# Optimization experiments

Hardware: AMD Instinct MI355X
Metric: run time of the kernel (lower is better)

The kernel has to match this reference:

```python
import jax, jax.numpy as jnp
import numpy as np

NUM_QUBITS = 4
QUANTUM_DEPTH = 2
BATCH = 1048576

# Hadamard matrix
_H = jnp.asarray(np.array([[1.0, 1.0], [1.0, -1.0]]) / np.sqrt(2.0), jnp.complex64)

# PauliZ sign table: signs[w, k] = +/-1 for basis state k on wire w (wire 0 = most significant axis)
_idx = np.arange(16)
_SIGNS = jnp.asarray(np.stack([1.0 - 2.0 * ((_idx >> (NUM_QUBITS - 1 - w)) & 1) for w in range(NUM_QUBITS)]), jnp.float32)  # (4,16)


def _apply_1q(state, U, w):
    # state: (B,2,2,2,2); apply 2x2 U on wire w
    a = 1 + w
    s = jnp.moveaxis(state, a, -1)
    s = s @ U.T  # new_j = sum_i U[j,i] * s[..., i]
    return jnp.moveaxis(s, -1, a)


def _apply_rz(state, theta, w):
    # diagonal RZ(theta) = diag(e^{-i t/2}, e^{i t/2}), theta: (B,)
    ph = jnp.exp(1j * jnp.stack([-theta / 2, theta / 2], axis=-1).astype(jnp.complex64))  # (B,2)
    shape = [state.shape[0], 1, 1, 1, 1]
    shape[1 + w] = 2
    return state * ph.reshape(shape)


def _cnot(state, c, t):
    ca, ta = 1 + c, 1 + t
    s0 = jnp.take(state, 0, axis=ca)
    s1 = jnp.take(state, 1, axis=ca)
    s1 = jnp.flip(s1, axis=ta if ta < ca else ta - 1)
    return jnp.stack([s0, s1], axis=ca)


def _ry_matrix(theta):
    c, s = jnp.cos(theta / 2), jnp.sin(theta / 2)
    return jnp.stack([jnp.stack([c, -s]), jnp.stack([s, c])]).astype(jnp.complex64)


def _simulate(inputs, params):
    B = inputs.shape[0]
    state = jnp.zeros((B, 2, 2, 2, 2), jnp.complex64).at[:, 0, 0, 0, 0].set(1.0)
    # feature map: H on all wires, RZ(inputs[:, w]), CNOT chain
    for w in range(NUM_QUBITS):
        state = _apply_1q(state, _H, w)
    for w in range(NUM_QUBITS):
        state = _apply_rz(state, inputs[:, w], w)
    for w in range(NUM_QUBITS - 1):
        state = _cnot(state, w, w + 1)
    # variational circuit
    for layer in range(QUANTUM_DEPTH):
        for w in range(NUM_QUBITS):
            state = _apply_1q(state, _ry_matrix(params[layer, w]), w)
        for w in range(NUM_QUBITS - 1):
            state = _cnot(state, w, w + 1)
        state = _cnot(state, NUM_QUBITS - 1, 0)
    probs = jnp.abs(state.reshape(B, 16)) ** 2  # (B,16) float32
    return probs @ _SIGNS.T  # (B,4) expvals of PauliZ per wire


def setup_inputs() -> dict:
    key = jax.random.key(0)
    k1, k2 = jax.random.split(key)
    inputs = jax.random.normal(k1, (BATCH, NUM_QUBITS), jnp.float32)
    params = jax.random.normal(k2, (QUANTUM_DEPTH, NUM_QUBITS), jnp.float32) * 0.1
    return {"inputs": inputs, "params": params}


def reference(inputs, params):
    return _simulate(inputs, params)
```

## Files before the change

### kernel.cpp

```cpp
#include <hip/hip_runtime.h>


typedef float v2f __attribute__((ext_vector_type(2)));

__global__ __launch_bounds__(256) void qsim_kernel(
    const float* __restrict__ inputs,
    const float* __restrict__ params,
    float* __restrict__ out,
    int B)
{
    int b = blockIdx.x * blockDim.x + threadIdx.x;
    if (b >= B) return;

    const float4 x4 = reinterpret_cast<const float4*>(inputs)[b];

    float cw[4], sw[4];
    __sincosf(0.5f * x4.x, &sw[0], &cw[0]);
    __sincosf(0.5f * x4.y, &sw[1], &cw[1]);
    __sincosf(0.5f * x4.z, &sw[2], &cw[2]);
    __sincosf(0.5f * x4.w, &sw[3], &cw[3]);

    v2f a[16];
    a[0] = (v2f){0.25f * cw[3], -0.25f * sw[3]};
    a[1] = (v2f){0.25f * cw[3],  0.25f * sw[3]};

    #pragma unroll
    for (int lvl = 0; lvl < 3; ++lvl) {
        const int w = 2 - lvl;
        const int st = 2 << lvl;
        const float c = cw[w], s = sw[w];
        #pragma unroll
        for (int j = 0; j < 8; ++j) {
            if (j < st) {
                const v2f v  = a[j];
                const v2f cv = v * c;
                const v2f sp = (v2f){-v.y, v.x} * s;
                a[j]      = cv - sp;
                a[j + st] = cv + sp;
            }
        }
    }

    auto cnot = [&](int cm, int tm) {
        #pragma unroll
        for (int j = 0; j < 16; ++j) {
            if ((j & cm) && !(j & tm)) {
                const int k = j | tm;
                v2f tmp = a[j]; a[j] = a[k]; a[k] = tmp;
            }
        }
    };

    auto ry = [&](int m, float c, float s) {
        #pragma unroll
        for (int j = 0; j < 16; ++j) {
            if (!(j & m)) {
                const int k = j | m;
                const v2f a0 = a[j], a1 = a[k];
                a[j] = a0 * c - a1 * s;
                a[k] = a0 * s + a1 * c;
            }
        }
    };

    cnot(8, 4); cnot(4, 2); cnot(2, 1);

    #pragma unroll
    for (int l = 0; l < 2; ++l) {
        float cp[4], sp[4];
        #pragma unroll
        for (int w = 0; w < 4; ++w)
            __sincosf(0.5f * params[l * 4 + w], &sp[w], &cp[w]);
        ry(8, cp[0], sp[0]);
        ry(4, cp[1], sp[1]);
        ry(2, cp[2], sp[2]);
        ry(1, cp[3], sp[3]);
        cnot(8, 4); cnot(4, 2); cnot(2, 1); cnot(1, 8);
    }

    v2f q[16];
    #pragma unroll
    for (int k = 0; k < 16; ++k) q[k] = a[k] * a[k];

    v2f t[8], o3v = (v2f){0.f, 0.f};
    #pragma unroll
    for (int j = 0; j < 8; ++j) {
        t[j] = q[2*j] + q[2*j+1];
        o3v += q[2*j] - q[2*j+1];
    }
    v2f u[4], o2v = (v2f){0.f, 0.f};
    #pragma unroll
    for (int j = 0; j < 4; ++j) {
        u[j] = t[2*j] + t[2*j+1];
        o2v += t[2*j] - t[2*j+1];
    }
    const v2f o1v = (u[0] - u[1]) + (u[2] - u[3]);
    const v2f o0v = (u[0] + u[1]) - (u[2] + u[3]);

    reinterpret_cast<float4*>(out)[b] =
        make_float4(o0v.x + o0v.y, o1v.x + o1v.y, o2v.x + o2v.y, o3v.x + o3v.y);
}

extern "C" void kernel_launch(void* const* d_in, const int* in_sizes, int n_in,
                              void* d_out, int out_size, void* d_ws, size_t ws_size,
                              hipStream_t stream) {
    const float* inputs = (const float*)d_in[0];
    const float* params = (const float*)d_in[1];
    float* out = (float*)d_out;
    const int B = in_sizes[0] / 4;
    const int threads = 256;
    const int blocks = (B + threads - 1) / threads;
    qsim_kernel<<<blocks, threads, 0, stream>>>(inputs, params, out, B);
}
```

Before: 79.75 us.

## Precompute parameter-only circuit into Fourier coefficient table, evaluate per-sample as trig polynomial

Adds a single-block prep kernel that builds the 16x16 unitary of the parameter-only part of the circuit. From it, the prep kernel derives a table of 81 float4 Fourier coefficients for the PauliZ expectations as functions of the input phases. The main kernel then computes per-sample phase products and sums coefficient-weighted cosines, instead of simulating the full 16-amplitude state per thread. This trades state-vector simulation work for an extra small launch and table reads from global memory. The prep kernel is still valid per call, since it reads params each time.

Result: faster. 75.99 us (-4.7%).

```diff
diff --git a/kernel.cpp b/kernel.cpp
--- a/kernel.cpp
+++ b/kernel.cpp
@@ -3,102 +3,133 @@
 
 typedef float v2f __attribute__((ext_vector_type(2)));
 
-__global__ __launch_bounds__(256) void qsim_kernel(
+__global__ void qprep_kernel(const float* __restrict__ params, float* __restrict__ tab) {
+    __shared__ float V[16][16];
+    __shared__ float4 T[81];
+    const int tid = threadIdx.x;
+    if (tid < 81) T[tid] = make_float4(0.f, 0.f, 0.f, 0.f);
+    if (tid < 16) {
+        float col[16];
+        #pragma unroll
+        for (int j = 0; j < 16; ++j) col[j] = (j == tid) ? 1.f : 0.f;
+        auto cnot = [&](int cm, int tm) {
+            #pragma unroll
+            for (int j = 0; j < 16; ++j)
+                if ((j & cm) && !(j & tm)) { int k = j | tm; float t0 = col[j]; col[j] = col[k]; col[k] = t0; }
+        };
+        auto ry = [&](int m, float c, float s) {
+            #pragma unroll
+            for (int j = 0; j < 16; ++j)
+                if (!(j & m)) { int k = j | m; float a0 = col[j], a1 = col[k]; col[j] = c*a0 - s*a1; col[k] = s*a0 + c*a1; }
+        };
+        cnot(8, 4); cnot(4, 2); cnot(2, 1);
+        #pragma unroll
+        for (int l = 0; l < 2; ++l) {
+            float cp[4], sp[4];
+            #pragma unroll
+            for (int w = 0; w < 4; ++w) __sincosf(0.5f * params[l*4 + w], &sp[w], &cp[w]);
+            ry(8, cp[0], sp[0]); ry(4, cp[1], sp[1]); ry(2, cp[2], sp[2]); ry(1, cp[3], sp[3]);
+            cnot(8, 4); cnot(4, 2); cnot(2, 1); cnot(1, 8);
+        }
+        #pragma unroll
+        for (int j = 0; j < 16; ++j) V[j][tid] = col[j];
+    }
+    __syncthreads();
+    for (int it = tid; it < 1024; it += 256) {
+        const int w = it >> 8, m = (it >> 4) & 15, mp = it & 15;
+        if (m == mp) continue;
+        int t = 0; int first = 1;
+        #pragma unroll
+        for (int u = 0; u < 4; ++u) {
+            const int d = ((m >> (3 - u)) & 1) - ((mp >> (3 - u)) & 1) + 1;
+            t = t * 3 + d;
+            if (first == 1 && d != 1) first = d;
+        }
+        if (first != 2) continue;
+        float g = 0.f;
+        #pragma unroll
+        for (int k = 0; k < 16; ++k) {
+            const float sgn = ((k >> (3 - w)) & 1) ? -1.f : 1.f;
+            g += sgn * V[k][m] * V[k][mp];
+        }
+        atomicAdd(((float*)&T[t]) + w, 0.125f * g);
+    }
+    __syncthreads();
+    if (tid < 81) reinterpret_cast<float4*>(tab)[tid] = T[tid];
+}
+
+__device__ __forceinline__ v2f cm2(v2f a, v2f bv, v2f br) { return a.x * bv + a.y * br; }
+
+__global__ __launch_bounds__(256) void qmain_kernel(
     const float* __restrict__ inputs,
-    const float* __restrict__ params,
+    const float4* __restrict__ tab,
     float* __restrict__ out,
     int B)
 {
-    int b = blockIdx.x * blockDim.x + threadIdx.x;
+    const int b = blockIdx.x * blockDim.x + threadIdx.x;
     if (b >= B) return;
+    const float4 x = reinterpret_cast<const float4*>(inputs)[b];
 
-    const float4 x4 = reinterpret_cast<const float4*>(inputs)[b];
+    v2f e[4], r[4], ec[4], rc[4];
+    {
+        float cc, ss;
+        __sincosf(x.x, &ss, &cc); e[0] = (v2f){cc, ss};
+        __sincosf(x.y, &ss, &cc); e[1] = (v2f){cc, ss};
+        __sincosf(x.z, &ss, &cc); e[2] = (v2f){cc, ss};
+        __sincosf(x.w, &ss, &cc); e[3] = (v2f){cc, ss};
+    }
+    #pragma unroll
+    for (int u = 0; u < 4; ++u) {
+        r[u]  = (v2f){-e[u].y, e[u].x};
+        ec[u] = (v2f){ e[u].x, -e[u].y};
+        rc[u] = (v2f){ e[u].y,  e[u].x};
+    }
 
-    float cw[4], sw[4];
-    __sincosf(0.5f * x4.x, &sw[0], &cw[0]);
-    __sincosf(0.5f * x4.y, &sw[1], &cw[1]);
-    __sincosf(0.5f * x4.z, &sw[2], &cw[2]);
-    __sincosf(0.5f * x4.w, &sw[3], &cw[3]);
-
-    v2f a[16];
-    a[0] = (v2f){0.25f * cw[3], -0.25f * sw[3]};
-    a[1] = (v2f){0.25f * cw[3],  0.25f * sw[3]};
-
+    v2f P2[9], P3[27];
     #pragma unroll
-    for (int lvl = 0; lvl < 3; ++lvl) {
-        const int w = 2 - lvl;
-        const int st = 2 << lvl;
-        const float c = cw[w], s = sw[w];
-        #pragma unroll
-        for (int j = 0; j < 8; ++j) {
-            if (j < st) {
-                const v2f v  = a[j];
-                const v2f cv = v * c;
-                const v2f sp = (v2f){-v.y, v.x} * s;
-                a[j]      = cv - sp;
-                a[j + st] = cv + sp;
-            }
+    for (int t = 0; t < 9; ++t) {
+        const int d0 = t / 3, d1 = t % 3;
+        if (d0 == 0 || (d0 == 1 && d1 == 0)) continue;
+        if (d0 == 1) P2[t] = (d1 == 1) ? (v2f){1.f, 0.f} : e[1];
+        else         P2[t] = (d1 == 1) ? e[0]
+                           : (d1 == 2) ? cm2(e[0], e[1], r[1])
+                                       : cm2(e[0], ec[1], rc[1]);
+    }
+    #pragma unroll
+    for (int t = 0; t < 27; ++t) {
+        const int d0 = t / 9, d1 = (t / 3) % 3, d2 = t % 3;
+        const bool ones01 = (d0 == 1 && d1 == 1);
+        if (d0 == 0 || (d0 == 1 && d1 == 0) || (ones01 && d2 == 0)) continue;
+        if (ones01) P3[t] = (d2 == 1) ? (v2f){1.f, 0.f} : e[2];
+        else {
+            const int tp = t / 3;
+            P3[t] = (d2 == 1) ? P2[tp]
+                  : (d2 == 2) ? cm2(P2[tp], e[2], r[2])
+                              : cm2(P2[tp], ec[2], rc[2]);
         }
     }
 
-    auto cnot = [&](int cm, int tm) {
-        #pragma unroll
-        for (int j = 0; j < 16; ++j) {
-            if ((j & cm) && !(j & tm)) {
-                const int k = j | tm;
-                v2f tmp = a[j]; a[j] = a[k]; a[k] = tmp;
-            }
+    v2f o01 = (v2f){0.f, 0.f}, o23 = (v2f){0.f, 0.f};
+    #pragma unroll
+    for (int t = 0; t < 81; ++t) {
+        const int d0 = t / 27, d1 = (t / 9) % 3, d2 = (t / 3) % 3, d3 = t % 3;
+        const int first = (d0 != 1) ? d0 : (d1 != 1) ? d1 : (d2 != 1) ? d2 : (d3 != 1) ? d3 : 1;
+        if (first != 2) continue;
+        const bool ones012 = (d0 == 1 && d1 == 1 && d2 == 1);
+        float cv;
+        if (ones012) cv = e[3].x;
+        else {
+            const int tp = t / 3;
+            if (d3 == 1)      cv = P3[tp].x;
+            else if (d3 == 2) cv = P3[tp].x * e[3].x - P3[tp].y * e[3].y;
+            else              cv = P3[tp].x * e[3].x + P3[tp].y * e[3].y;
         }
-    };
-
-    auto ry = [&](int m, float c, float s) {
-        #pragma unroll
-        for (int j = 0; j < 16; ++j) {
-            if (!(j & m)) {
-                const int k = j | m;
-                const v2f a0 = a[j], a1 = a[k];
-                a[j] = a0 * c - a1 * s;
-                a[k] = a0 * s + a1 * c;
-            }
-        }
-    };
-
-    cnot(8, 4); cnot(4, 2); cnot(2, 1);
-
-    #pragma unroll
-    for (int l = 0; l < 2; ++l) {
-        float cp[4], sp[4];
-        #pragma unroll
-        for (int w = 0; w < 4; ++w)
-            __sincosf(0.5f * params[l * 4 + w], &sp[w], &cp[w]);
-        ry(8, cp[0], sp[0]);
-        ry(4, cp[1], sp[1]);
-        ry(2, cp[2], sp[2]);
-        ry(1, cp[3], sp[3]);
-        cnot(8, 4); cnot(4, 2); cnot(2, 1); cnot(1, 8);
+        const float4 cf = tab[t];
+        o01 += cv * (v2f){cf.x, cf.y};
+        o23 += cv * (v2f){cf.z, cf.w};
     }
 
-    v2f q[16];
-    #pragma unroll
-    for (int k = 0; k < 16; ++k) q[k] = a[k] * a[k];
-
-    v2f t[8], o3v = (v2f){0.f, 0.f};
-    #pragma unroll
-    for (int j = 0; j < 8; ++j) {
-        t[j] = q[2*j] + q[2*j+1];
-        o3v += q[2*j] - q[2*j+1];
-    }
-    v2f u[4], o2v = (v2f){0.f, 0.f};
-    #pragma unroll
-    for (int j = 0; j < 4; ++j) {
-        u[j] = t[2*j] + t[2*j+1];
-        o2v += t[2*j] - t[2*j+1];
-    }
-    const v2f o1v = (u[0] - u[1]) + (u[2] - u[3]);
-    const v2f o0v = (u[0] + u[1]) - (u[2] + u[3]);
-
-    reinterpret_cast<float4*>(out)[b] =
-        make_float4(o0v.x + o0v.y, o1v.x + o1v.y, o2v.x + o2v.y, o3v.x + o3v.y);
+    reinterpret_cast<float4*>(out)[b] = make_float4(o01.x, o01.y, o23.x, o23.y);
 }
 
 extern "C" void kernel_launch(void* const* d_in, const int* in_sizes, int n_in,
@@ -107,8 +138,11 @@
     const float* inputs = (const float*)d_in[0];
     const float* params = (const float*)d_in[1];
     float* out = (float*)d_out;
+    float* tab = (float*)d_ws;
     const int B = in_sizes[0] / 4;
+
+    qprep_kernel<<<1, 256, 0, stream>>>(params, tab);
     const int threads = 256;
     const int blocks = (B + threads - 1) / threads;
-    qsim_kernel<<<blocks, threads, 0, stream>>>(inputs, params, out, B);
+    qmain_kernel<<<blocks, threads, 0, stream>>>(inputs, (const float4*)tab, out, B);
 }
```
